# Kernel tuning notes

Measured on AMD Instinct MI355X. Metric: run time of the kernel, lower is better.

## Reference

```python
import jax, jax.numpy as jnp
import numpy as np

EMBED_DIM = 1024
N_HEADS = 16
HEAD_DIM = EMBED_DIM // N_HEADS


def setup_inputs() -> dict:
    key = jax.random.key(0)
    ks = jax.random.split(key, 8)
    B, Tq, Tk, C = 2, 2048, 2048, EMBED_DIM
    s = 1.0 / np.sqrt(C)
    return {
        "query": jax.random.normal(ks[0], (B, Tq, C), jnp.float32),
        "context": jax.random.normal(ks[1], (B, Tk, C), jnp.float32),
        "Wq": jax.random.normal(ks[2], (C, C), jnp.float32) * s,
        "bq": jnp.zeros((C,), jnp.float32),
        "Wkv": jax.random.normal(ks[3], (C, 2 * C), jnp.float32) * s,
        "bkv": jnp.zeros((2 * C,), jnp.float32),
        "Wo": jax.random.normal(ks[4], (C, C), jnp.float32) * s,
        "bo": jnp.zeros((C,), jnp.float32),
    }


def reference(query, context, Wq, bq, Wkv, bkv, Wo, bo):
    B, Tq, C = query.shape
    Tk = context.shape[1]
    H, D = N_HEADS, HEAD_DIM
    # projections
    q = (query @ Wq + bq).reshape(B, Tq, H, D)        # [B,Tq,H,D]
    kv = (context @ Wkv + bkv).reshape(B, Tk, 2, H, D)
    k = kv[:, :, 0]                                   # [B,Tk,H,D]
    v = kv[:, :, 1]
    scale = D ** -0.5
    # attention scores [B,H,Tq,Tk]
    attn = jnp.einsum("bqhd,bkhd->bhqk", q, k) * scale
    attn = jax.nn.softmax(attn, axis=-1)
    # dropout p=0.0 -> identity in eval / p=0
    out = jnp.einsum("bhqk,bkhd->bqhd", attn, v).reshape(B, Tq, C)
    return out @ Wo + bo
```

## Files before the change

kernel.cpp:

```cpp
#include <hip/hip_runtime.h>
#include <math.h>

typedef unsigned short u16;
typedef unsigned int u32;
typedef __attribute__((ext_vector_type(8))) short short8;
typedef __attribute__((ext_vector_type(4))) short short4v;
typedef __attribute__((ext_vector_type(4))) float f32x4;

__device__ __forceinline__ u16 f2bf(float f) {
  union { float f; unsigned u; } x; x.f = f;
  unsigned r = x.u + 0x7FFFu + ((x.u >> 16) & 1u);
  return (u16)(r >> 16);
}

__device__ __forceinline__ u32 asu(float f) {
  union { float f; u32 u; } x; x.f = f; return x.u;
}

__device__ __forceinline__ u32 pack2bf(float a, float b) {
  return __builtin_amdgcn_perm(asu(b) + 0x8000u, asu(a) + 0x8000u, 0x07060302u);
}

__device__ __forceinline__ u32 cvtpk2bf(float a, float b) {
  u32 r;
  asm("v_cvt_pk_bf16_f32 %0, %1, %2" : "=v"(r) : "v"(a), "v"(b));
  return r;
}

__device__ __forceinline__ void gld_lds16(const void* g, void* l) {
  __builtin_amdgcn_global_load_lds(
      (const __attribute__((address_space(1))) unsigned int*)g,
      (__attribute__((address_space(3))) unsigned int*)l, 16, 0, 0);
}

__global__ void pre_kernel(const float* __restrict__ q, const float* __restrict__ c,
                           const float* __restrict__ Wq, const float* __restrict__ Wkv,
                           const float* __restrict__ Wo,
                           u16* __restrict__ xq, u16* __restrict__ xc,
                           u16* __restrict__ WqF, u16* __restrict__ WkvF,
                           u16* __restrict__ WoF) {
  __shared__ float tile[32][33];
  int bx = blockIdx.x;
  int t = threadIdx.y * 32 + threadIdx.x;
  if (bx < 8192) {
    int i = bx * 256 + t;
    const float* src = q; u16* dst = xq;
    if (i >= 1048576) { i -= 1048576; src = c; dst = xc; }
    float4 v = ((const float4*)src)[i];
    ((uint2*)dst)[i] = make_uint2(
        (unsigned)f2bf(v.x) | ((unsigned)f2bf(v.y) << 16),
        (unsigned)f2bf(v.z) | ((unsigned)f2bf(v.w) << 16));
  } else {
    int g = bx - 8192;
    int gx = g & 127, gy = g >> 7;
    const float* src; u16* dst; int N, n0;
    if (gx < 32)      { src = Wq;  dst = WqF;  N = 1024; n0 = gx * 32; }
    else if (gx < 96) { src = Wkv; dst = WkvF; N = 2048; n0 = (gx - 32) * 32; }
    else              { src = Wo;  dst = WoF;  N = 1024; n0 = (gx - 96) * 32; }
    int k0 = gy * 32;
    int tx = threadIdx.x, ty = threadIdx.y;
#pragma unroll
    for (int i = 0; i < 4; ++i)
      tile[ty * 4 + i][tx] = src[(size_t)(k0 + ty * 4 + i) * N + n0 + tx];
    __syncthreads();
    int e = t * 4;
    int ch = e >> 9, rem = e & 511;
    int kg = (rem >> 7) & 3;
    int nl = (rem >> 3) & 15;
    int j0 = rem & 7;
    int kk = kg * 8 + j0;
    int nn = ch * 16 + nl;
    u32 lo = pack2bf(tile[kk][nn], tile[kk + 1][nn]);
    u32 hi = pack2bf(tile[kk + 2][nn], tile[kk + 3][nn]);
    *(uint2*)(dst + (size_t)(((n0 >> 4) + ch) * 32 + gy) * 512 + rem) = make_uint2(lo, hi);
  }
}

__global__ __launch_bounds__(256, 3) void qkv_gemm(
    const u16* __restrict__ Xq, const u16* __restrict__ Xc,
    const u16* __restrict__ WqF, const u16* __restrict__ WkvF,
    const float* __restrict__ bq, const float* __restrict__ bkv,
    u16* __restrict__ qb, u16* __restrict__ kf, u16* __restrict__ vf,
    float qscale) {
  __shared__ __align__(16) u16 smem[16896];
  const int tid = threadIdx.x, lane = tid & 63, wave = tid >> 6;
  const int quad = lane >> 4, cl = lane & 15;
  const int wr = (wave >> 1) * 64, wc = (wave & 1) * 64;

  const int xcd = blockIdx.x & 7, pos = blockIdx.x >> 3;
  const u16 *A, *Bf; const float* bias; int m0, n0; bool isq;
  if (pos < 64) {
    isq = false; A = Xc; Bf = WkvF; bias = bkv;
    m0 = ((xcd >> 1) * 8 + (pos >> 3)) * 128;
    n0 = ((xcd & 1) * 8 + (pos & 7)) * 128;
  } else {
    int p = pos - 64;
    isq = true;  A = Xq; Bf = WqF;  bias = bq;
    m0 = (xcd * 4 + (p >> 3)) * 128;
    n0 = (p & 7) * 128;
  }
  const int bn4 = (n0 + wc) >> 4;

  const int rA = lane >> 3;
  const int kcs = ((lane & 7) ^ rA) * 8;
  const int r7 = cl & 7;

  auto stageA = [&](int k0, int buf) {
    u16* As = smem + buf * 8192;
#pragma unroll
    for (int it = 0; it < 4; ++it) {
      int chunk = it * 4 + wave;
      gld_lds16(A + (size_t)(m0 + chunk * 8 + rA) * 1024 + k0 + kcs, As + chunk * 512);
    }
  };

  f32x4 acc[4][4] = {};
  short8 bA[2][4], bB[2][4];

  auto loadB = [&](short8 (&dst)[2][4], int k05) {
#pragma unroll
    for (int ks = 0; ks < 2; ++ks)
#pragma unroll
      for (int ni = 0; ni < 4; ++ni)
        dst[ks][ni] = *(const short8*)(Bf + (size_t)((bn4 + ni) * 32 + k05 + ks) * 512 + lane * 8);
  };

  auto compute = [&](const u16* As, short8 (&breg)[2][4]) {
#pragma unroll
    for (int ks = 0; ks < 2; ++ks) {
      short8 af[4];
#pragma unroll
      for (int mi = 0; mi < 4; ++mi) {
        int row = wr + mi * 16 + cl;
        af[mi] = *(const short8*)(As + (row >> 3) * 512 + r7 * 64 +
                                  (((ks << 2) | quad) ^ r7) * 8);
      }
#pragma unroll
      for (int mi = 0; mi < 4; ++mi)
#pragma unroll
        for (int ni = 0; ni < 4; ++ni)
          acc[mi][ni] = __builtin_amdgcn_mfma_f32_16x16x32_bf16(af[mi], breg[ks][ni], acc[mi][ni], 0, 0, 0);
    }
  };

  stageA(0, 0);
  loadB(bA, 0);
  __syncthreads();

#pragma unroll 1
  for (int ii = 0; ii < 8; ++ii) {
    const int i = ii * 2;
    stageA((i + 1) * 64, 1);
    loadB(bB, (i + 1) * 2);
    compute(smem, bA);
    __syncthreads();
    const int j = i + 1;
    if (j < 15) { stageA((j + 1) * 64, 0); loadB(bA, (j + 1) * 2); }
    compute(smem + 8192, bB);
    __syncthreads();
  }

  if (isq) {
#pragma unroll
    for (int mi = 0; mi < 4; ++mi)
#pragma unroll
      for (int ni = 0; ni < 4; ++ni)
#pragma unroll
        for (int r = 0; r < 4; ++r) {
          int row = m0 + wr + mi * 16 + quad * 4 + r;
          int col = n0 + wc + ni * 16 + cl;
          qb[(size_t)row * 1024 + col] = f2bf((acc[mi][ni][r] + bias[col]) * qscale);
        }
    return;
  }

  const int b = m0 >> 11, kt0 = (m0 & 2047) >> 6;
  const bool kreg = (n0 < 1024);
  if (kreg) {
#pragma unroll
    for (int mi = 0; mi < 4; ++mi)
#pragma unroll
      for (int ni = 0; ni < 4; ++ni)
#pragma unroll
        for (int r = 0; r < 4; ++r)
          smem[(wr + mi * 16 + quad * 4 + r) * 132 + wc + ni * 16 + cl] =
              f2bf(acc[mi][ni][r] + bias[n0 + wc + ni * 16 + cl]);
    __syncthreads();
#pragma unroll
    for (int i = 0; i < 8; ++i) {
      int c = i * 4 + wave;
      int hs = c >> 4, ts = (c >> 3) & 1, ks = (c >> 2) & 1, idx = c & 3;
      int h = (n0 >> 6) + hs;
      size_t bhkt = ((size_t)((b * 16 + h) * 32 + kt0 + ts)) * 4096;
      short8 v = *(const short8*)(smem + (ts * 64 + idx * 16 + cl) * 132 +
                                  hs * 64 + ks * 32 + quad * 8);
      *(short8*)(kf + bhkt + (size_t)(ks * 4 + idx) * 512 + lane * 8) = v;
    }
  } else {
#pragma unroll
    for (int mi = 0; mi < 4; ++mi)
#pragma unroll
      for (int ni = 0; ni < 4; ++ni) {
        float v0 = acc[mi][ni][0] + bias[n0 + wc + ni * 16 + cl];
        float v1 = acc[mi][ni][1] + bias[n0 + wc + ni * 16 + cl];
        float v2 = acc[mi][ni][2] + bias[n0 + wc + ni * 16 + cl];
        float v3 = acc[mi][ni][3] + bias[n0 + wc + ni * 16 + cl];
        *(uint2*)(smem + (wc + ni * 16 + cl) * 132 + wr + mi * 16 + quad * 4) =
            make_uint2(pack2bf(v0, v1), pack2bf(v2, v3));
      }
    __syncthreads();
#pragma unroll
    for (int i = 0; i < 8; ++i) {
      int c = i * 4 + wave;
      int hs = c >> 4, ts = (c >> 3) & 1, ks = (c >> 2) & 1, idx = c & 3;
      int h = ((n0 - 1024) >> 6) + hs;
      size_t bhkt = ((size_t)((b * 16 + h) * 32 + kt0 + ts)) * 4096;
      const u16* src = smem + (hs * 64 + idx * 16 + cl) * 132 + ts * 64 + ks * 32 + quad * 4;
      short8 v;
      *(short4v*)&v       = *(const short4v*)(src);
      *((short4v*)&v + 1) = *(const short4v*)(src + 16);
      *(short8*)(vf + bhkt + (size_t)(ks * 4 + idx) * 512 + lane * 8) = v;
    }
  }
}

__global__ __launch_bounds__(256) void o_gemm(
    const u16* __restrict__ A, const u16* __restrict__ Bf,
    const float* __restrict__ bias, float* __restrict__ Cm) {
  __shared__ __align__(16) u16 smem[24576];
  const int tid = threadIdx.x, lane = tid & 63, wave = tid >> 6;
  const int quad = lane >> 4, cl = lane & 15;
  const int xcd = blockIdx.x & 7, pos = blockIdx.x >> 3;
  const int m0 = (xcd * 8 + (pos >> 3)) * 64, n0 = (pos & 7) * 128;
  const int wr = (wave >> 1) * 32, wc = (wave & 1) * 64;
  const int n04 = n0 >> 4;

  const int rA = lane >> 3;
  const int kcs = ((lane & 7) ^ rA) * 8;
  const int r7 = cl & 7;

  auto stageA = [&](int k0, int buf) {
    u16* As = smem + buf * 4096;
#pragma unroll
    for (int it = 0; it < 2; ++it) {
      int chunk = wave * 2 + it;
      gld_lds16(A + (size_t)(m0 + chunk * 8 + rA) * 1024 + k0 + kcs, As + chunk * 512);
    }
  };
  auto stageB = [&](int k0, int buf) {
    u16* Bs = smem + 8192 + buf * 8192;
    const int k05 = k0 >> 5;
#pragma unroll
    for (int it = 0; it < 4; ++it) {
      int c = it * 4 + wave;
      int j = c >> 1, ks = c & 1;
      gld_lds16(Bf + (size_t)((n04 + j) * 32 + k05 + ks) * 512 + lane * 8, Bs + c * 512);
    }
  };

  f32x4 acc[2][4] = {};

  stageA(0, 0);
  stageB(0, 0);
  __syncthreads();

  for (int i = 0; i < 16; ++i) {
    const int k0 = i * 64;
    const int cur = i & 1;
    if (i < 15) { stageA(k0 + 64, cur ^ 1); stageB(k0 + 64, cur ^ 1); }
    const u16* As = smem + cur * 4096;
    const u16* Bs = smem + 8192 + cur * 8192;
    short8 bf[2][4];
#pragma unroll
    for (int ks = 0; ks < 2; ++ks)
#pragma unroll
      for (int ni = 0; ni < 4; ++ni)
        bf[ks][ni] = *(const short8*)(Bs + (size_t)((((wave & 1) * 4 + ni) * 2 + ks) * 512) + lane * 8);
#pragma unroll
    for (int ks = 0; ks < 2; ++ks) {
      short8 af[2];
#pragma unroll
      for (int mi = 0; mi < 2; ++mi) {
        int row = wr + mi * 16 + cl;
        af[mi] = *(const short8*)(As + (row >> 3) * 512 + r7 * 64 +
                                  (((ks << 2) | quad) ^ r7) * 8);
      }
#pragma unroll
      for (int mi = 0; mi < 2; ++mi)
#pragma unroll
        for (int ni = 0; ni < 4; ++ni)
          acc[mi][ni] = __builtin_amdgcn_mfma_f32_16x16x32_bf16(af[mi], bf[ks][ni], acc[mi][ni], 0, 0, 0);
    }
    __syncthreads();
  }
#pragma unroll
  for (int mi = 0; mi < 2; ++mi)
#pragma unroll
    for (int ni = 0; ni < 4; ++ni)
#pragma unroll
      for (int r = 0; r < 4; ++r) {
        int row = m0 + wr + mi * 16 + quad * 4 + r;
        int col = n0 + wc + ni * 16 + cl;
        Cm[(size_t)row * 1024 + col] = acc[mi][ni][r] + bias[col];
      }
}

__global__ __launch_bounds__(256, 2) void flash_attn(
    const u16* __restrict__ qb, const u16* __restrict__ kf,
    const u16* __restrict__ vf, u16* __restrict__ outp) {
  __shared__ __align__(16) u16 kv[2][16 * 512];
  const int tid = threadIdx.x, lane = tid & 63, wave = tid >> 6;
  const int quad = lane >> 4, cl = lane & 15;
  const int id = blockIdx.x;
  const int h = (id & 7) | (((id >> 3) & 1) << 3);
  const int b = (id >> 4) & 1;
  const int qt = id >> 5;

  const int qrow0 = b * 2048 + qt * 128 + wave * 32;
  short8 bq0[2], bq1[2];
#pragma unroll
  for (int ks = 0; ks < 2; ++ks) {
    bq0[ks] = *(const short8*)(qb + (size_t)(qrow0 + cl) * 1024 + h * 64 + ks * 32 + quad * 8);
    bq1[ks] = *(const short8*)(qb + (size_t)(qrow0 + 16 + cl) * 1024 + h * 64 + ks * 32 + quad * 8);
  }

  short8 ones;
#pragma unroll
  for (int j = 0; j < 8; ++j) ones[j] = (short)0x3F80;

  const u16* kfb = kf + (size_t)((b * 16 + h) * 32) * 4096;
  const u16* vfb = vf + (size_t)((b * 16 + h) * 32) * 4096;

  auto stage = [&](int kt, int buf) {
#pragma unroll
    for (int i = 0; i < 4; ++i) {
      int c = wave * 4 + i;
      const u16* src = (c < 8) ? (kfb + (size_t)kt * 4096 + c * 512)
                               : (vfb + (size_t)kt * 4096 + (c - 8) * 512);
      gld_lds16(src + lane * 8, &kv[buf][c * 512]);
    }
  };

  f32x4 o0[4] = {}, o1[4] = {};
  f32x4 l0 = {}, l1 = {};

  stage(0, 0);
  __syncthreads();

#pragma unroll 1
  for (int kt = 0; kt < 32; ++kt) {
    const int cur = kt & 1;
    if (kt < 31) stage(kt + 1, cur ^ 1);
    const u16* kb = &kv[cur][0];
    const u16* vb = &kv[cur][8 * 512];
    f32x4 s0[4] = {}, s1[4] = {};
    __builtin_amdgcn_s_setprio(1);
#pragma unroll
    for (int ks = 0; ks < 2; ++ks)
#pragma unroll
      for (int ni = 0; ni < 4; ++ni) {
        short8 ak = *(const short8*)(kb + (ks * 4 + ni) * 512 + lane * 8);
        s0[ni] = __builtin_amdgcn_mfma_f32_16x16x32_bf16(ak, bq0[ks], s0[ni], 0, 0, 0);
        s1[ni] = __builtin_amdgcn_mfma_f32_16x16x32_bf16(ak, bq1[ks], s1[ni], 0, 0, 0);
      }
    __builtin_amdgcn_s_setprio(0);
    short8 av[2][4];
#pragma unroll
    for (int ks = 0; ks < 2; ++ks)
#pragma unroll
      for (int nd = 0; nd < 4; ++nd)
        av[ks][nd] = *(const short8*)(vb + (ks * 4 + nd) * 512 + lane * 8);
    u32 bp0[2][4], bp1[2][4];
#pragma unroll
    for (int ni = 0; ni < 4; ++ni) {
      float a0 = __builtin_amdgcn_exp2f(s0[ni][0]);
      float a1 = __builtin_amdgcn_exp2f(s0[ni][1]);
      float a2 = __builtin_amdgcn_exp2f(s0[ni][2]);
      float a3 = __builtin_amdgcn_exp2f(s0[ni][3]);
      bp0[ni >> 1][(ni & 1) * 2 + 0] = cvtpk2bf(a0, a1);
      bp0[ni >> 1][(ni & 1) * 2 + 1] = cvtpk2bf(a2, a3);
      float c0 = __builtin_amdgcn_exp2f(s1[ni][0]);
      float c1 = __builtin_amdgcn_exp2f(s1[ni][1]);
      float c2 = __builtin_amdgcn_exp2f(s1[ni][2]);
      float c3 = __builtin_amdgcn_exp2f(s1[ni][3]);
      bp1[ni >> 1][(ni & 1) * 2 + 0] = cvtpk2bf(c0, c1);
      bp1[ni >> 1][(ni & 1) * 2 + 1] = cvtpk2bf(c2, c3);
    }
    __builtin_amdgcn_s_setprio(1);
#pragma unroll
    for (int ks = 0; ks < 2; ++ks) {
      short8 pb0, pb1;
      *(u32*)&pb0     = bp0[ks][0];
      ((u32*)&pb0)[1] = bp0[ks][1];
      ((u32*)&pb0)[2] = bp0[ks][2];
      ((u32*)&pb0)[3] = bp0[ks][3];
      *(u32*)&pb1     = bp1[ks][0];
      ((u32*)&pb1)[1] = bp1[ks][1];
      ((u32*)&pb1)[2] = bp1[ks][2];
      ((u32*)&pb1)[3] = bp1[ks][3];
#pragma unroll
      for (int nd = 0; nd < 4; ++nd) {
        o0[nd] = __builtin_amdgcn_mfma_f32_16x16x32_bf16(av[ks][nd], pb0, o0[nd], 0, 0, 0);
        o1[nd] = __builtin_amdgcn_mfma_f32_16x16x32_bf16(av[ks][nd], pb1, o1[nd], 0, 0, 0);
      }
      l0 = __builtin_amdgcn_mfma_f32_16x16x32_bf16(ones, pb0, l0, 0, 0, 0);
      l1 = __builtin_amdgcn_mfma_f32_16x16x32_bf16(ones, pb1, l1, 0, 0, 0);
    }
    __builtin_amdgcn_s_setprio(0);
    __syncthreads();
  }
  float inv0 = 1.f / l0[0], inv1 = 1.f / l1[0];
  u16* Ow = &kv[0][wave * 32 * 68];
#pragma unroll
  for (int nd = 0; nd < 4; ++nd)
#pragma unroll
    for (int r2 = 0; r2 < 2; ++r2) {
      *(u32*)(Ow + cl * 68 + nd * 16 + quad * 4 + r2 * 2) =
          cvtpk2bf(o0[nd][r2 * 2] * inv0, o0[nd][r2 * 2 + 1] * inv0);
      *(u32*)(Ow + (16 + cl) * 68 + nd * 16 + quad * 4 + r2 * 2) =
          cvtpk2bf(o1[nd][r2 * 2] * inv1, o1[nd][r2 * 2 + 1] * inv1);
    }
#pragma unroll
  for (int p = 0; p < 4; ++p) {
    int row = p * 8 + (lane >> 3);
    int d0 = (lane & 7) * 8;
    short8 ov = *(const short8*)(Ow + row * 68 + d0);
    *(short8*)(outp + (size_t)(qrow0 + row) * 1024 + h * 64 + d0) = ov;
  }
}

extern "C" void kernel_launch(void* const* d_in, const int* in_sizes, int n_in,
                              void* d_out, int out_size, void* d_ws, size_t ws_size,
                              hipStream_t stream) {
  const float* query   = (const float*)d_in[0];
  const float* context = (const float*)d_in[1];
  const float* Wq  = (const float*)d_in[2];
  const float* bq  = (const float*)d_in[3];
  const float* Wkv = (const float*)d_in[4];
  const float* bkv = (const float*)d_in[5];
  const float* Wo  = (const float*)d_in[6];
  const float* bo  = (const float*)d_in[7];
  float* out = (float*)d_out;

  char* ws = (char*)d_ws;
  size_t off = 0;
  auto alloc = [&](size_t bytes) {
    char* p = ws + off;
    off += (bytes + 255) & ~(size_t)255;
    return p;
  };
  u16* buf0 = (u16*)alloc(4096ull * 1024 * 2);
  u16* xcb  = (u16*)alloc(4096ull * 1024 * 2);
  u16* WqF  = (u16*)alloc(1024ull * 1024 * 2);
  u16* WkvF = (u16*)alloc(2048ull * 1024 * 2);
  u16* WoF  = (u16*)alloc(1024ull * 1024 * 2);
  u16* qb   = (u16*)alloc(4096ull * 1024 * 2);
  u16* kfr  = (u16*)alloc(4ull * 1024 * 1024 * 2);
  u16* vfr  = (u16*)alloc(4ull * 1024 * 1024 * 2);

  const float QSCALE = 0.125f * 1.44269504f;

  pre_kernel<<<12288, dim3(32, 8), 0, stream>>>(query, context, Wq, Wkv, Wo,
                                                buf0, xcb, WqF, WkvF, WoF);
  qkv_gemm<<<768, 256, 0, stream>>>(buf0, xcb, WqF, WkvF, bq, bkv,
                                    qb, kfr, vfr, QSCALE);
  flash_attn<<<512, 256, 0, stream>>>(qb, kfr, vfr, buf0);
  o_gemm<<<512, 256, 0, stream>>>(buf0, WoF, bo, out);
}
```

Baseline: 182.3 us.

## Process two KV tiles per pipeline stage in flash attention

Doubles the LDS staging buffer so each double-buffered stage loads two consecutive 64-key K/V tiles, which halves the number of loop iterations and __syncthreads barriers. Both QK^T products are issued before the two softmax/PV phases, giving the scheduler more independent MFMA work to overlap with the exp2 and LDS reads. LDS use per block grows to 64 KB, and two sets of score accumulators raise register pressure, which may hurt occupancy under the 2-blocks-per-CU launch bound.

```diff
diff --git a/kernel.cpp b/kernel.cpp
--- a/kernel.cpp
+++ b/kernel.cpp
@@ -308,7 +308,7 @@
 __global__ __launch_bounds__(256, 2) void flash_attn(
     const u16* __restrict__ qb, const u16* __restrict__ kf,
     const u16* __restrict__ vf, u16* __restrict__ outp) {
-  __shared__ __align__(16) u16 kv[2][16 * 512];
+  __shared__ __align__(16) u16 kv[2][32 * 512];
   const int tid = threadIdx.x, lane = tid & 63, wave = tid >> 6;
   const int quad = lane >> 4, cl = lane & 15;
   const int id = blockIdx.x;
@@ -331,45 +331,41 @@
   const u16* kfb = kf + (size_t)((b * 16 + h) * 32) * 4096;
   const u16* vfb = vf + (size_t)((b * 16 + h) * 32) * 4096;
 
-  auto stage = [&](int kt, int buf) {
-#pragma unroll
-    for (int i = 0; i < 4; ++i) {
-      int c = wave * 4 + i;
-      const u16* src = (c < 8) ? (kfb + (size_t)kt * 4096 + c * 512)
-                               : (vfb + (size_t)kt * 4096 + (c - 8) * 512);
-      gld_lds16(src + lane * 8, &kv[buf][c * 512]);
+  auto stage = [&](int p, int buf) {
+#pragma unroll
+    for (int i = 0; i < 8; ++i) {
+      int c = wave * 8 + i;
+      int half = c >> 4;
+      int sub = (c >> 3) & 1;
+      int ch = c & 7;
+      const u16* base = half ? vfb : kfb;
+      gld_lds16(base + (size_t)(p * 2 + sub) * 4096 + ch * 512 + lane * 8,
+                &kv[buf][(size_t)c * 512]);
     }
   };
 
   f32x4 o0[4] = {}, o1[4] = {};
   f32x4 l0 = {}, l1 = {};
 
-  stage(0, 0);
-  __syncthreads();
-
-#pragma unroll 1
-  for (int kt = 0; kt < 32; ++kt) {
-    const int cur = kt & 1;
-    if (kt < 31) stage(kt + 1, cur ^ 1);
-    const u16* kb = &kv[cur][0];
-    const u16* vb = &kv[cur][8 * 512];
-    f32x4 s0[4] = {}, s1[4] = {};
+  auto qk = [&](const u16* kbase, f32x4 (&s0)[4], f32x4 (&s1)[4]) {
     __builtin_amdgcn_s_setprio(1);
 #pragma unroll
     for (int ks = 0; ks < 2; ++ks)
 #pragma unroll
       for (int ni = 0; ni < 4; ++ni) {
-        short8 ak = *(const short8*)(kb + (ks * 4 + ni) * 512 + lane * 8);
+        short8 ak = *(const short8*)(kbase + (ks * 4 + ni) * 512 + lane * 8);
         s0[ni] = __builtin_amdgcn_mfma_f32_16x16x32_bf16(ak, bq0[ks], s0[ni], 0, 0, 0);
         s1[ni] = __builtin_amdgcn_mfma_f32_16x16x32_bf16(ak, bq1[ks], s1[ni], 0, 0, 0);
       }
     __builtin_amdgcn_s_setprio(0);
+  };
+  auto softpv = [&](const u16* vbase, f32x4 (&s0)[4], f32x4 (&s1)[4]) {
     short8 av[2][4];
 #pragma unroll
     for (int ks = 0; ks < 2; ++ks)
 #pragma unroll
       for (int nd = 0; nd < 4; ++nd)
-        av[ks][nd] = *(const short8*)(vb + (ks * 4 + nd) * 512 + lane * 8);
+        av[ks][nd] = *(const short8*)(vbase + (ks * 4 + nd) * 512 + lane * 8);
     u32 bp0[2][4], bp1[2][4];
 #pragma unroll
     for (int ni = 0; ni < 4; ++ni) {
@@ -407,6 +403,22 @@
       l1 = __builtin_amdgcn_mfma_f32_16x16x32_bf16(ones, pb1, l1, 0, 0, 0);
     }
     __builtin_amdgcn_s_setprio(0);
+  };
+
+  stage(0, 0);
+  __syncthreads();
+
+#pragma unroll 1
+  for (int p = 0; p < 16; ++p) {
+    const int cur = p & 1;
+    if (p < 15) stage(p + 1, cur ^ 1);
+    const u16* base = &kv[cur][0];
+    f32x4 sA0[4] = {}, sA1[4] = {};
+    f32x4 sB0[4] = {}, sB1[4] = {};
+    qk(base, sA0, sA1);
+    qk(base + 8 * 512, sB0, sB1);
+    softpv(base + 16 * 512, sA0, sA1);
+    softpv(base + 24 * 512, sB0, sB1);
     __syncthreads();
   }
   float inv0 = 1.f / l0[0], inv1 = 1.f / l1[0];
```

Result: no change. 182.1 us (-0.1%).

## Load o_gemm B fragments directly to registers, shrink LDS for higher occupancy

Applied to the files above, without the earlier changes.

The output-projection GEMM no longer stages pre-swizzled B tiles through shared memory. Each wave loads its own B fragments from global memory straight into registers, double-buffered across a manually unrolled k loop. Only the A tile stays in LDS, which cuts LDS use to 16 KB, and the launch bounds now request 3 blocks per SM. The cost is more register pressure and redundant global reads of B across the waves that share columns.

```diff
diff --git a/kernel.cpp b/kernel.cpp
--- a/kernel.cpp
+++ b/kernel.cpp
@@ -224,58 +224,41 @@
   }
 }
 
-__global__ __launch_bounds__(256) void o_gemm(
+__global__ __launch_bounds__(256, 3) void o_gemm(
     const u16* __restrict__ A, const u16* __restrict__ Bf,
     const float* __restrict__ bias, float* __restrict__ Cm) {
-  __shared__ __align__(16) u16 smem[24576];
+  __shared__ __align__(16) u16 As2[2][4096];
   const int tid = threadIdx.x, lane = tid & 63, wave = tid >> 6;
   const int quad = lane >> 4, cl = lane & 15;
   const int xcd = blockIdx.x & 7, pos = blockIdx.x >> 3;
   const int m0 = (xcd * 8 + (pos >> 3)) * 64, n0 = (pos & 7) * 128;
   const int wr = (wave >> 1) * 32, wc = (wave & 1) * 64;
-  const int n04 = n0 >> 4;
+  const int bn4 = (n0 + wc) >> 4;
 
   const int rA = lane >> 3;
   const int kcs = ((lane & 7) ^ rA) * 8;
   const int r7 = cl & 7;
 
   auto stageA = [&](int k0, int buf) {
-    u16* As = smem + buf * 4096;
 #pragma unroll
     for (int it = 0; it < 2; ++it) {
       int chunk = wave * 2 + it;
-      gld_lds16(A + (size_t)(m0 + chunk * 8 + rA) * 1024 + k0 + kcs, As + chunk * 512);
-    }
-  };
-  auto stageB = [&](int k0, int buf) {
-    u16* Bs = smem + 8192 + buf * 8192;
-    const int k05 = k0 >> 5;
-#pragma unroll
-    for (int it = 0; it < 4; ++it) {
-      int c = it * 4 + wave;
-      int j = c >> 1, ks = c & 1;
-      gld_lds16(Bf + (size_t)((n04 + j) * 32 + k05 + ks) * 512 + lane * 8, Bs + c * 512);
+      gld_lds16(A + (size_t)(m0 + chunk * 8 + rA) * 1024 + k0 + kcs, As2[buf] + chunk * 512);
     }
   };
 
   f32x4 acc[2][4] = {};
-
-  stageA(0, 0);
-  stageB(0, 0);
-  __syncthreads();
-
-  for (int i = 0; i < 16; ++i) {
-    const int k0 = i * 64;
-    const int cur = i & 1;
-    if (i < 15) { stageA(k0 + 64, cur ^ 1); stageB(k0 + 64, cur ^ 1); }
-    const u16* As = smem + cur * 4096;
-    const u16* Bs = smem + 8192 + cur * 8192;
-    short8 bf[2][4];
+  short8 bA[2][4], bB[2][4];
+
+  auto loadB = [&](short8 (&dst)[2][4], int k05) {
 #pragma unroll
     for (int ks = 0; ks < 2; ++ks)
 #pragma unroll
       for (int ni = 0; ni < 4; ++ni)
-        bf[ks][ni] = *(const short8*)(Bs + (size_t)((((wave & 1) * 4 + ni) * 2 + ks) * 512) + lane * 8);
+        dst[ks][ni] = *(const short8*)(Bf + (size_t)((bn4 + ni) * 32 + k05 + ks) * 512 + lane * 8);
+  };
+
+  auto compute = [&](const u16* As, short8 (&breg)[2][4]) {
 #pragma unroll
     for (int ks = 0; ks < 2; ++ks) {
       short8 af[2];
@@ -289,8 +272,24 @@
       for (int mi = 0; mi < 2; ++mi)
 #pragma unroll
         for (int ni = 0; ni < 4; ++ni)
-          acc[mi][ni] = __builtin_amdgcn_mfma_f32_16x16x32_bf16(af[mi], bf[ks][ni], acc[mi][ni], 0, 0, 0);
-    }
+          acc[mi][ni] = __builtin_amdgcn_mfma_f32_16x16x32_bf16(af[mi], breg[ks][ni], acc[mi][ni], 0, 0, 0);
+    }
+  };
+
+  stageA(0, 0);
+  loadB(bA, 0);
+  __syncthreads();
+
+#pragma unroll 1
+  for (int ii = 0; ii < 8; ++ii) {
+    const int i = ii * 2;
+    stageA((i + 1) * 64, 1);
+    loadB(bB, (i + 1) * 2);
+    compute(As2[0], bA);
+    __syncthreads();
+    const int j = i + 1;
+    if (j < 15) { stageA((j + 1) * 64, 0); loadB(bA, (j + 1) * 2); }
+    compute(As2[1], bB);
     __syncthreads();
   }
 #pragma unroll
```

Result: slower. 190.9 us (+4.7%).
